# Performance work log

Hardware: AMD Instinct MI355X
Metric: run time of the kernel (lower is better)

## Reference

```python
import jax, jax.numpy as jnp
import numpy as np

EPS = 1e-5   # BatchNorm3d eps
SLOPE = 0.01 # LeakyReLU default negative_slope

def conv3(x, w, pad):
    return jax.lax.conv_general_dilated(
        x, w, (1, 1, 1), [(pad, pad)] * 3,
        dimension_numbers=('NCDHW', 'OIDHW', 'NCDHW'))

def bn(x):
    # BatchNorm3d in training mode with affine init (weight=1, bias=0):
    # normalize by per-channel batch statistics (biased variance).
    m = x.mean(axis=(0, 2, 3, 4), keepdims=True)
    v = x.var(axis=(0, 2, 3, 4), keepdims=True)
    return (x - m) / jnp.sqrt(v + EPS)

def lrelu(x):
    return jnp.where(x >= 0, x, SLOPE * x)

def block(x, w1, w2):
    # ConvBlock: conv3x3x3 -> BN -> LeakyReLU, twice
    x = lrelu(bn(conv3(x, w1, 1)))
    return lrelu(bn(conv3(x, w2, 1)))

def maxpool2(x):
    # MaxPool3dMPS(kernel=2, stride=2, pad=0) == standard 2x2x2 maxpool
    B, C, D, H, W = x.shape
    return x.reshape(B, C, D // 2, 2, H // 2, 2, W // 2, 2).max(axis=(3, 5, 7))

def upconv_fft(x, w):
    # ConvTranspose3dMPS: nearest-neighbor upsample by stride=2 via repeat,
    # then per-(out,in)-channel CIRCULAR convolution implemented with FFTs
    # (weight zero-padded to the upsampled spatial shape). Vectorized here
    # over all channel pairs with a frequency-domain einsum; rfft is used
    # since all signals are real (identical math, half the memory).
    s = 2
    B, C, D, H, W = x.shape
    up = jnp.broadcast_to(x[:, :, :, None, :, None, :, None],
                          (B, C, D, s, H, s, W, s)).reshape(B, C, D * s, H * s, W * s)
    sp = up.shape[2:]
    X = jnp.fft.rfftn(up, axes=(2, 3, 4))                 # [B, Cin, D', H', Wf]
    Wf = jnp.fft.rfftn(w, s=sp, axes=(2, 3, 4))           # [Cout, Cin, D', H', Wf]
    Y = jnp.einsum('bidhw,oidhw->bodhw', X, Wf)
    return jnp.fft.irfftn(Y, s=sp, axes=(2, 3, 4))

def unet_fwd(x, wf1, wf2, wd1a, wd1b, wd2a, wd2b, wd3a, wd3b,
             wt1, wu1a, wu1b, wt2, wu2a, wu2b, wt3, wu3a, wu3b,
             w_final, b_final):
    x1 = block(x, wf1, wf2)                       # [B,16,64,64,64]
    x2 = block(maxpool2(x1), wd1a, wd1b)          # [B,32,32,32,32]
    x3 = block(maxpool2(x2), wd2a, wd2b)          # [B,64,16,16,16]
    x4 = block(maxpool2(x3), wd3a, wd3b)          # [B,128,8,8,8]

    def up(a, skip, wt, wa, wb):
        u = lrelu(bn(upconv_fft(a, wt)))
        return block(jnp.concatenate([skip, u], axis=1), wa, wb)

    a = up(x4, x3, wt1, wu1a, wu1b)               # [B,64,16,16,16]
    a = up(a, x2, wt2, wu2a, wu2b)                # [B,32,32,32,32]
    a = up(a, x1, wt3, wu3a, wu3b)                # [B,16,64,64,64]
    return conv3(a, w_final, 0) + b_final.reshape(1, -1, 1, 1, 1)

def setup_inputs() -> dict:
    key = jax.random.key(0)
    ks = jax.random.split(key, 32)
    def W(k, shape):
        fan = int(np.prod(shape[1:]))
        return jax.random.normal(k, shape, jnp.float32) * np.float32((2.0 / fan) ** 0.5)
    inp = {}
    inp['x'] = jax.random.normal(ks[0], (1, 1, 64, 64, 64), jnp.float32)
    shapes = {
        'wf1': (16, 1, 3, 3, 3),  'wf2': (16, 16, 3, 3, 3),
        'wd1a': (32, 16, 3, 3, 3), 'wd1b': (32, 32, 3, 3, 3),
        'wd2a': (64, 32, 3, 3, 3), 'wd2b': (64, 64, 3, 3, 3),
        'wd3a': (128, 64, 3, 3, 3), 'wd3b': (128, 128, 3, 3, 3),
        'wt1': (64, 128, 2, 2, 2), 'wu1a': (64, 128, 3, 3, 3), 'wu1b': (64, 64, 3, 3, 3),
        'wt2': (32, 64, 2, 2, 2),  'wu2a': (32, 64, 3, 3, 3),  'wu2b': (32, 32, 3, 3, 3),
        'wt3': (16, 32, 2, 2, 2),  'wu3a': (16, 32, 3, 3, 3),  'wu3b': (16, 16, 3, 3, 3),
        'w_final': (1, 16, 1, 1, 1),
    }
    for i, (name, sh) in enumerate(shapes.items()):
        inp[name] = W(ks[i + 1], sh)
    inp['b_final'] = jnp.zeros((1,), jnp.float32)
    return inp

def reference(x, wf1, wf2, wd1a, wd1b, wd2a, wd2b, wd3a, wd3b,
              wt1, wu1a, wu1b, wt2, wu2a, wu2b, wt3, wu3a, wu3b,
              w_final, b_final):
    return unet_fwd(x, wf1, wf2, wd1a, wd1b, wd2a, wd2b, wd3a, wd3b,
                    wt1, wu1a, wu1b, wt2, wu2a, wu2b, wt3, wu3a, wu3b,
                    w_final, b_final)
```

## Files before the change

kernel.cpp:

```cpp
#include <hip/hip_runtime.h>

#define EPS   1e-5f
#define SLOPE 0.01f

template <int CIN>
__global__ __launch_bounds__(64) void conv3_big(const float* __restrict__ in,
                                                const float* __restrict__ wt,
                                                float* __restrict__ out,
                                                float* __restrict__ bstat) {
    const int V   = 64 * 64 * 64;
    const int NB  = gridDim.y;
    const int co0 = blockIdx.x * 8;
    __shared__ float tile[3][6][68];

    const int vb    = blockIdx.y * 256;
    const int d0    = vb >> 12;
    const int hbase = (vb >> 6) & 63;
    const int hh0   = threadIdx.x >> 4;
    const int w0    = (threadIdx.x & 15) * 4;
    const int v0    = vb + (hh0 * 64) + w0;
    const bool mL = (w0 != 0);
    const bool mR = (w0 + 4 != 64);

    int  goff[5];
    int  loff[5];
    bool gok[5];
    bool act[5];
#pragma unroll
    for (int t = 0; t < 5; ++t) {
        const int idx = threadIdx.x + t * 64;
        act[t] = (idx < 288);
        const int r  = idx >> 4;
        const int wq = (idx & 15) * 4;
        const int kd = r / 6;
        const int hh = r - kd * 6;
        const int zd = d0 + kd - 1;
        const int zh = hbase + hh - 1;
        gok[t]  = act[t] & ((unsigned)zd < 64u) & ((unsigned)zh < 64u);
        goff[t] = gok[t] ? ((zd << 6) + zh) * 64 + wq : 0;
        loff[t] = act[t] ? (kd * 6 + hh) * 68 + wq : 0;
    }

    float acc[32];
#pragma unroll
    for (int i = 0; i < 32; ++i) acc[i] = 0.f;

    float4 pre[5];
#pragma unroll
    for (int t = 0; t < 5; ++t) {
        float4 val = make_float4(0.f, 0.f, 0.f, 0.f);
        if (gok[t]) val = *(const float4*)(in + goff[t]);
        pre[t] = val;
    }

#pragma unroll 1
    for (int ci = 0; ci < CIN; ++ci) {
#pragma unroll
        for (int t = 0; t < 5; ++t)
            if (act[t]) *(float4*)&((float*)tile)[loff[t]] = pre[t];
        if (ci + 1 < CIN) {
            const float* pc = in + (size_t)(ci + 1) * V;
#pragma unroll
            for (int t = 0; t < 5; ++t) {
                float4 val = make_float4(0.f, 0.f, 0.f, 0.f);
                if (gok[t]) val = *(const float4*)(pc + goff[t]);
                pre[t] = val;
            }
        }
#pragma unroll 1
        for (int kd = 0; kd < 3; ++kd) {
#pragma unroll
            for (int kh = 0; kh < 3; ++kh) {
                const float* trow = &tile[kd][hh0 + kh][0];
                const float4 m = *(const float4*)(trow + w0);
                const float lv = mL ? trow[w0 - 1] : 0.f;
                const float rv = mR ? trow[w0 + 4] : 0.f;
                const float* wbase = wt + ((size_t)co0 * CIN + ci) * 27
                                        + (kd * 3 + kh) * 3;
#define FMA4C(A0, A1, A2, AP)                                                       \
                {                                                                   \
                    float* a = (AP);                                                \
                    a[0] = fmaf(lv,  (A0), fmaf(m.x, (A1), fmaf(m.y, (A2), a[0]))); \
                    a[1] = fmaf(m.x, (A0), fmaf(m.y, (A1), fmaf(m.z, (A2), a[1]))); \
                    a[2] = fmaf(m.y, (A0), fmaf(m.z, (A1), fmaf(m.w, (A2), a[2]))); \
                    a[3] = fmaf(m.z, (A0), fmaf(m.w, (A1), fmaf(rv,  (A2), a[3]))); \
                }
#pragma unroll
                for (int co = 0; co < 8; ++co) {
                    const float* wp = wbase + (size_t)co * (CIN * 27);
                    const float a0 = wp[0];
                    const float a1 = wp[1];
                    const float a2 = wp[2];
                    FMA4C(a0, a1, a2, acc + co * 4);
                }
#undef FMA4C
            }
        }
    }
#pragma unroll
    for (int co = 0; co < 8; ++co)
        *(float4*)&out[(size_t)(co0 + co) * V + v0] = *(const float4*)&acc[co * 4];

    float s1[8], s2[8];
#pragma unroll
    for (int co = 0; co < 8; ++co) {
        const float* a = &acc[co * 4];
        s1[co] = a[0] + a[1] + a[2] + a[3];
        s2[co] = fmaf(a[0], a[0], fmaf(a[1], a[1], fmaf(a[2], a[2], a[3] * a[3])));
    }
#pragma unroll
    for (int off = 32; off > 0; off >>= 1)
#pragma unroll
        for (int co = 0; co < 8; ++co) {
            s1[co] += __shfl_down(s1[co], off, 64);
            s2[co] += __shfl_down(s2[co], off, 64);
        }
    if (threadIdx.x == 0)
#pragma unroll
        for (int co = 0; co < 8; ++co) {
            bstat[((size_t)(co0 + co) * NB + blockIdx.y) * 2]     = s1[co];
            bstat[((size_t)(co0 + co) * NB + blockIdx.y) * 2 + 1] = s2[co];
        }
}

template <int CIN, int CC>
__global__ __launch_bounds__(128) void conv3_t32(const float* __restrict__ in,
                                                 const float* __restrict__ wt,
                                                 float* __restrict__ part) {
    const int V    = 32 * 32 * 32;
    const int Cout = gridDim.x * 8;
    const int z    = blockIdx.z;
    const int cib  = z * CC;
    __shared__ float wlds[27 * CC * 8];
    __shared__ float tile[3][18][36];
    const int co0 = blockIdx.x * 8;
    for (int i = threadIdx.x; i < 27 * CC * 8; i += 128) {
        const int co  = i & 7;
        const int r   = i >> 3;
        const int tap = r % 3;
        const int r2  = r / 3;
        const int pl  = r2 % 9;
        const int ci  = r2 / 9;
        wlds[i] = wt[((size_t)(co0 + co) * CIN + cib + ci) * 27 + pl * 3 + tap];
    }

    const int vb    = blockIdx.y * 512;
    const int d0    = vb >> 10;
    const int hbase = (vb >> 5) & 31;
    const int hh0   = threadIdx.x >> 3;
    const int w0    = (threadIdx.x & 7) * 4;
    const int v0    = vb + hh0 * 32 + w0;
    const bool mL = (w0 != 0);
    const bool mR = (w0 + 4 != 32);

    int  goff[4];
    int  loff[4];
    bool gok[4];
    bool act[4];
#pragma unroll
    for (int t = 0; t < 4; ++t) {
        const int idx = threadIdx.x + t * 128;
        act[t] = (idx < 432);
        const int r  = idx >> 3;
        const int wq = (idx & 7) * 4;
        const int kd = r / 18;
        const int hh = r - kd * 18;
        const int zd = d0 + kd - 1;
        const int zh = hbase + hh - 1;
        gok[t]  = act[t] & ((unsigned)zd < 32u) & ((unsigned)zh < 32u);
        goff[t] = gok[t] ? ((zd << 5) + zh) * 32 + wq : 0;
        loff[t] = act[t] ? (kd * 18 + hh) * 36 + wq : 0;
    }

    float acc[32];
#pragma unroll
    for (int i = 0; i < 32; ++i) acc[i] = 0.f;

    const float* inz = in + (size_t)cib * V;
    float4 pre[4];
#pragma unroll
    for (int t = 0; t < 4; ++t) {
        float4 val = make_float4(0.f, 0.f, 0.f, 0.f);
        if (gok[t]) val = *(const float4*)(inz + goff[t]);
        pre[t] = val;
    }

#pragma unroll 1
    for (int ci = 0; ci < CC; ++ci) {
        __syncthreads();
#pragma unroll
        for (int t = 0; t < 4; ++t)
            if (act[t]) *(float4*)&((float*)tile)[loff[t]] = pre[t];
        if (ci + 1 < CC) {
            const float* pc = inz + (size_t)(ci + 1) * V;
#pragma unroll
            for (int t = 0; t < 4; ++t) {
                float4 val = make_float4(0.f, 0.f, 0.f, 0.f);
                if (gok[t]) val = *(const float4*)(pc + goff[t]);
                pre[t] = val;
            }
        }
        __syncthreads();
#pragma unroll 1
        for (int kd = 0; kd < 3; ++kd) {
#pragma unroll
            for (int kh = 0; kh < 3; ++kh) {
                const float* trow = &tile[kd][hh0 + kh][0];
                const float4 m = *(const float4*)(trow + w0);
                const float lv = mL ? trow[w0 - 1] : 0.f;
                const float rv = mR ? trow[w0 + 4] : 0.f;
                const float* wb = &wlds[((ci * 9 + kd * 3 + kh) * 3) * 8];
                const float4 t0a = *(const float4*)(wb);
                const float4 t0b = *(const float4*)(wb + 4);
                const float4 t1a = *(const float4*)(wb + 8);
                const float4 t1b = *(const float4*)(wb + 12);
                const float4 t2a = *(const float4*)(wb + 16);
                const float4 t2b = *(const float4*)(wb + 20);
#define FMA4C(A0, A1, A2, AP)                                                       \
                {                                                                   \
                    float* a = (AP);                                                \
                    a[0] = fmaf(lv,  (A0), fmaf(m.x, (A1), fmaf(m.y, (A2), a[0]))); \
                    a[1] = fmaf(m.x, (A0), fmaf(m.y, (A1), fmaf(m.z, (A2), a[1]))); \
                    a[2] = fmaf(m.y, (A0), fmaf(m.z, (A1), fmaf(m.w, (A2), a[2]))); \
                    a[3] = fmaf(m.z, (A0), fmaf(m.w, (A1), fmaf(rv,  (A2), a[3]))); \
                }
                FMA4C(t0a.x, t1a.x, t2a.x, acc + 0);
                FMA4C(t0a.y, t1a.y, t2a.y, acc + 4);
                FMA4C(t0a.z, t1a.z, t2a.z, acc + 8);
                FMA4C(t0a.w, t1a.w, t2a.w, acc + 12);
                FMA4C(t0b.x, t1b.x, t2b.x, acc + 16);
                FMA4C(t0b.y, t1b.y, t2b.y, acc + 20);
                FMA4C(t0b.z, t1b.z, t2b.z, acc + 24);
                FMA4C(t0b.w, t1b.w, t2b.w, acc + 28);
#undef FMA4C
            }
        }
    }
#pragma unroll
    for (int co = 0; co < 8; ++co)
        *(float4*)&part[((size_t)z * Cout + co0 + co) * V + v0] = *(const float4*)&acc[co * 4];
}

template <int CIN>
__global__ __launch_bounds__(256) void upconv_big(const float* __restrict__ in,
                                                  const float* __restrict__ wt,
                                                  float* __restrict__ out,
                                                  float* __restrict__ bstat,
                                                  int Di, int Hi, int Wi) {
    const int Do = 2 * Di, Ho = 2 * Hi, Wo = 2 * Wi;
    const int Vo = Do * Ho * Wo;
    const int Vi = Di * Hi * Wi;
    const int NB = gridDim.y;
    const int co0 = blockIdx.x * 8;
    __shared__ float wlds[8 * CIN * 8];
    __shared__ float sred[4 * 16];
    for (int i = threadIdx.x; i < 8 * CIN * 8; i += 256) {
        const int co  = i & 7;
        const int t2  = i >> 3;
        const int ci  = t2 % CIN;
        const int tap = t2 / CIN;
        wlds[i] = wt[((size_t)(co0 + co) * CIN + ci) * 8 + tap];
    }
    __syncthreads();

    const int vbase = blockIdx.y * 1024 + threadIdx.x;
    int od[4], oh[4], ow[4];
#pragma unroll
    for (int j = 0; j < 4; ++j) {
        const int v = vbase + j * 256;
        ow[j] = v % Wo;
        oh[j] = (v / Wo) % Ho;
        od[j] = v / (Wo * Ho);
    }
    float acc[32];
#pragma unroll
    for (int i = 0; i < 32; ++i) acc[i] = 0.f;

#pragma unroll 1
    for (int kd = 0; kd < 2; ++kd)
#pragma unroll 1
    for (int kh = 0; kh < 2; ++kh)
#pragma unroll
    for (int kw = 0; kw < 2; ++kw) {
        const int tap = (kd * 2 + kh) * 2 + kw;
        int sp[4];
#pragma unroll
        for (int j = 0; j < 4; ++j) {
            const int id = ((od[j] - kd + Do) & (Do - 1)) >> 1;
            const int ih = ((oh[j] - kh + Ho) & (Ho - 1)) >> 1;
            const int iw = ((ow[j] - kw + Wo) & (Wo - 1)) >> 1;
            sp[j] = (id * Hi + ih) * Wi + iw;
        }
        const float* wrow = &wlds[tap * CIN * 8];
#pragma unroll 2
        for (int ci = 0; ci < CIN; ++ci) {
            float xv[4];
#pragma unroll
            for (int j = 0; j < 4; ++j)
                xv[j] = in[(size_t)ci * Vi + sp[j]];
            const float4 wa = *(const float4*)(wrow + ci * 8);
            const float4 wb = *(const float4*)(wrow + ci * 8 + 4);
#define UF(WC, CO)                                                              \
            {                                                                   \
                _Pragma("unroll")                                               \
                for (int j = 0; j < 4; ++j)                                     \
                    acc[(CO) * 4 + j] = fmaf(xv[j], (WC), acc[(CO) * 4 + j]);   \
            }
            UF(wa.x, 0) UF(wa.y, 1) UF(wa.z, 2) UF(wa.w, 3)
            UF(wb.x, 4) UF(wb.y, 5) UF(wb.z, 6) UF(wb.w, 7)
#undef UF
        }
    }
#pragma unroll
    for (int co = 0; co < 8; ++co)
#pragma unroll
        for (int j = 0; j < 4; ++j)
            out[(size_t)(co0 + co) * Vo + vbase + j * 256] = acc[co * 4 + j];

    float s1[8], s2[8];
#pragma unroll
    for (int co = 0; co < 8; ++co) {
        const float* a = &acc[co * 4];
        s1[co] = a[0] + a[1] + a[2] + a[3];
        s2[co] = fmaf(a[0], a[0], fmaf(a[1], a[1], fmaf(a[2], a[2], a[3] * a[3])));
    }
#pragma unroll
    for (int off = 32; off > 0; off >>= 1)
#pragma unroll
        for (int co = 0; co < 8; ++co) {
            s1[co] += __shfl_down(s1[co], off, 64);
            s2[co] += __shfl_down(s2[co], off, 64);
        }
    const int lane = threadIdx.x & 63;
    const int wv   = threadIdx.x >> 6;
    if (lane == 0)
#pragma unroll
        for (int co = 0; co < 8; ++co) {
            sred[(wv * 8 + co) * 2]     = s1[co];
            sred[(wv * 8 + co) * 2 + 1] = s2[co];
        }
    __syncthreads();
    if ((int)threadIdx.x < 8) {
        float S1 = 0.f, S2 = 0.f;
#pragma unroll
        for (int w = 0; w < 4; ++w) {
            S1 += sred[(w * 8 + threadIdx.x) * 2];
            S2 += sred[(w * 8 + threadIdx.x) * 2 + 1];
        }
        bstat[((size_t)(co0 + threadIdx.x) * NB + blockIdx.y) * 2]     = S1;
        bstat[((size_t)(co0 + threadIdx.x) * NB + blockIdx.y) * 2 + 1] = S2;
    }
}

__global__ __launch_bounds__(256) void bn_apply_f(const float* __restrict__ prt,
                                                  float* __restrict__ dst,
                                                  const float* __restrict__ bstat,
                                                  int NB, int V4, float invV) {
    const int c = blockIdx.x;
    float s1 = 0.f, s2 = 0.f;
    for (int i = threadIdx.x; i < NB; i += 256) {
        s1 += bstat[((size_t)c * NB + i) * 2];
        s2 += bstat[((size_t)c * NB + i) * 2 + 1];
    }
#pragma unroll
    for (int off = 32; off > 0; off >>= 1) {
        s1 += __shfl_down(s1, off, 64);
        s2 += __shfl_down(s2, off, 64);
    }
    __shared__ float sh[8];
    __shared__ float mv[2];
    const int lane = threadIdx.x & 63;
    const int wv   = threadIdx.x >> 6;
    if (lane == 0) { sh[wv] = s1; sh[4 + wv] = s2; }
    __syncthreads();
    if (threadIdx.x == 0) {
        const float S1 = sh[0] + sh[1] + sh[2] + sh[3];
        const float S2 = sh[4] + sh[5] + sh[6] + sh[7];
        const float mean = S1 * invV;
        const float var  = S2 * invV - mean * mean;
        mv[0] = mean;
        mv[1] = rsqrtf(var + EPS);
    }
    __syncthreads();
    const float mean = mv[0];
    const float rstd = mv[1];
    const int pos = blockIdx.y * 256 + threadIdx.x;
    float4 t = ((const float4*)prt)[(size_t)c * V4 + pos];
    float u;
    u = (t.x - mean) * rstd; t.x = u >= 0.f ? u : SLOPE * u;
    u = (t.y - mean) * rstd; t.y = u >= 0.f ? u : SLOPE * u;
    u = (t.z - mean) * rstd; t.z = u >= 0.f ? u : SLOPE * u;
    u = (t.w - mean) * rstd; t.w = u >= 0.f ? u : SLOPE * u;
    ((float4*)dst)[(size_t)c * V4 + pos] = t;
}

template <int CIN, int CC, int BT>
__global__ __launch_bounds__(BT) void conv3_qA(const float* __restrict__ in,
                                               const float* __restrict__ wt,
                                               float* __restrict__ part,
                                               int D, int H, int W) {
    const int V    = D * H * W;
    const int Cout = gridDim.x * 8;
    const int z    = blockIdx.z;
    const int cib  = z * CC;
    __shared__ float wlds[27 * CC * 8];
    const int co0 = blockIdx.x * 8;
    for (int i = threadIdx.x; i < 27 * CC * 8; i += BT) {
        const int co  = i & 7;
        const int t2  = i >> 3;
        const int tap = t2 % 3;
        const int t3  = t2 / 3;
        const int ci  = t3 % CC;
        const int pl  = t3 / CC;
        wlds[i] = wt[((size_t)(co0 + co) * CIN + cib + ci) * 27 + pl * 3 + tap];
    }
    __syncthreads();

    const float* inz = in + (size_t)cib * V;
    const int v0 = (blockIdx.y * BT + threadIdx.x) * 4;
    const int w0 = v0 % W;
    const int h0 = (v0 / W) % H;
    const int d0 = v0 / (W * H);

    const bool mL = (w0 != 0);
    const bool mR = (w0 + 4 != W);
    const int  wl = w0 - (mL ? 1 : 0);
    const int  wr = w0 + (mR ? 4 : 3);

    float acc[32];
#pragma unroll
    for (int i = 0; i < 32; ++i) acc[i] = 0.f;

#pragma unroll 1
    for (int kd = 0; kd < 3; ++kd) {
#pragma unroll 1
        for (int kh = 0; kh < 3; ++kh) {
            const int zd = d0 + kd - 1, zh = h0 + kh - 1;
            const bool okp = ((unsigned)zd < (unsigned)D) & ((unsigned)zh < (unsigned)H);
            const int row = okp ? (zd * H + zh) * W : 0;
            const float* wpl = &wlds[(kd * 3 + kh) * CC * 24];
#pragma unroll 2
            for (int ci = 0; ci < CC; ++ci) {
                const float* p = inz + (size_t)ci * V + row;
                float4 m = *(const float4*)(p + w0);
                float lv = p[wl];
                float rv = p[wr];
                if (!okp) { m.x = 0.f; m.y = 0.f; m.z = 0.f; m.w = 0.f; }
                if (!(okp && mL)) lv = 0.f;
                if (!(okp && mR)) rv = 0.f;
                const float* wb = wpl + ci * 24;
                const float4 t0a = *(const float4*)(wb);
                const float4 t0b = *(const float4*)(wb + 4);
                const float4 t1a = *(const float4*)(wb + 8);
                const float4 t1b = *(const float4*)(wb + 12);
                const float4 t2a = *(const float4*)(wb + 16);
                const float4 t2b = *(const float4*)(wb + 20);
#define FMA4C(A0, A1, A2, AP)                                                       \
                {                                                                   \
                    float* a = (AP);                                                \
                    a[0] = fmaf(lv,  (A0), fmaf(m.x, (A1), fmaf(m.y, (A2), a[0]))); \
                    a[1] = fmaf(m.x, (A0), fmaf(m.y, (A1), fmaf(m.z, (A2), a[1]))); \
                    a[2] = fmaf(m.y, (A0), fmaf(m.z, (A1), fmaf(m.w, (A2), a[2]))); \
                    a[3] = fmaf(m.z, (A0), fmaf(m.w, (A1), fmaf(rv,  (A2), a[3]))); \
                }
                FMA4C(t0a.x, t1a.x, t2a.x, acc + 0);
                FMA4C(t0a.y, t1a.y, t2a.y, acc + 4);
                FMA4C(t0a.z, t1a.z, t2a.z, acc + 8);
                FMA4C(t0a.w, t1a.w, t2a.w, acc + 12);
                FMA4C(t0b.x, t1b.x, t2b.x, acc + 16);
                FMA4C(t0b.y, t1b.y, t2b.y, acc + 20);
                FMA4C(t0b.z, t1b.z, t2b.z, acc + 24);
                FMA4C(t0b.w, t1b.w, t2b.w, acc + 28);
#undef FMA4C
            }
        }
    }
#pragma unroll
    for (int co = 0; co < 8; ++co)
        *(float4*)&part[((size_t)z * Cout + co0 + co) * V + v0] = *(const float4*)&acc[co * 4];
}

template <int CIN, int CC, int VOXB>
__global__ __launch_bounds__(256) void upconv_v8(const float* __restrict__ in,
                                                 const float* __restrict__ wt,
                                                 float* __restrict__ part,
                                                 int Di, int Hi, int Wi) {
    const int Do = 2 * Di, Ho = 2 * Hi, Wo = 2 * Wi;
    const int Vo = Do * Ho * Wo;
    const int Vi = Di * Hi * Wi;
    const int Cout = gridDim.x * 8;
    const int z    = blockIdx.z;
    const int cib  = z * CC;
    __shared__ float wlds[8 * CC * 8];
    const int co0 = blockIdx.x * 8;
    for (int i = threadIdx.x; i < 8 * CC * 8; i += 256) {
        const int co  = i & 7;
        const int t2  = i >> 3;
        const int ci  = t2 % CC;
        const int tap = t2 / CC;
        wlds[i] = wt[((size_t)(co0 + co) * CIN + cib + ci) * 8 + tap];
    }
    __syncthreads();

    const float* inz = in + (size_t)cib * Vi;
    const int vbase = blockIdx.y * (256 * VOXB) + threadIdx.x;
    int od[VOXB], oh[VOXB], ow[VOXB];
#pragma unroll
    for (int j = 0; j < VOXB; ++j) {
        const int v = vbase + j * 256;
        ow[j] = v % Wo;
        oh[j] = (v / Wo) % Ho;
        od[j] = v / (Wo * Ho);
    }
    float acc[8 * VOXB];
#pragma unroll
    for (int i = 0; i < 8 * VOXB; ++i) acc[i] = 0.f;

#pragma unroll 1
    for (int kd = 0; kd < 2; ++kd)
#pragma unroll 1
    for (int kh = 0; kh < 2; ++kh)
#pragma unroll
    for (int kw = 0; kw < 2; ++kw) {
        const int tap = (kd * 2 + kh) * 2 + kw;
        int sp[VOXB];
#pragma unroll
        for (int j = 0; j < VOXB; ++j) {
            const int id = ((od[j] - kd + Do) & (Do - 1)) >> 1;
            const int ih = ((oh[j] - kh + Ho) & (Ho - 1)) >> 1;
            const int iw = ((ow[j] - kw + Wo) & (Wo - 1)) >> 1;
            sp[j] = (id * Hi + ih) * Wi + iw;
        }
        const float* wrow = &wlds[tap * CC * 8];
#pragma unroll 2
        for (int ci = 0; ci < CC; ++ci) {
            float xv[VOXB];
#pragma unroll
            for (int j = 0; j < VOXB; ++j)
                xv[j] = inz[(size_t)ci * Vi + sp[j]];
            const float4 wa = *(const float4*)(wrow + ci * 8);
            const float4 wb = *(const float4*)(wrow + ci * 8 + 4);
#define UF(WC, CO)                                                              \
            {                                                                   \
                _Pragma("unroll")                                               \
                for (int j = 0; j < VOXB; ++j)                                  \
                    acc[(CO) * VOXB + j] = fmaf(xv[j], (WC), acc[(CO) * VOXB + j]); \
            }
            UF(wa.x, 0) UF(wa.y, 1) UF(wa.z, 2) UF(wa.w, 3)
            UF(wb.x, 4) UF(wb.y, 5) UF(wb.z, 6) UF(wb.w, 7)
#undef UF
        }
    }
#pragma unroll
    for (int co = 0; co < 8; ++co)
#pragma unroll
        for (int j = 0; j < VOXB; ++j)
            part[((size_t)z * Cout + co0 + co) * Vo + vbase + j * 256] = acc[co * VOXB + j];
}

__global__ __launch_bounds__(256) void bn_stats_part_v2(const float* __restrict__ part,
                                                        float* __restrict__ pstat,
                                                        int C, int V, int S, int chunk) {
    const int c = blockIdx.x, seg = blockIdx.y;
    const size_t base = (size_t)c * V + (size_t)seg * chunk;
    float s1 = 0.f, s2 = 0.f;
    for (int i = threadIdx.x * 4; i < chunk; i += 1024) {
        float4 t = make_float4(0.f, 0.f, 0.f, 0.f);
        for (int s = 0; s < S; ++s) {
            const float4 v = *(const float4*)(part + (size_t)s * C * V + base + i);
            t.x += v.x; t.y += v.y; t.z += v.z; t.w += v.w;
        }
        s1 += t.x + t.y + t.z + t.w;
        s2 = fmaf(t.x, t.x, fmaf(t.y, t.y, fmaf(t.z, t.z, fmaf(t.w, t.w, s2))));
    }
#pragma unroll
    for (int off = 32; off > 0; off >>= 1) {
        s1 += __shfl_down(s1, off, 64);
        s2 += __shfl_down(s2, off, 64);
    }
    __shared__ float sh[8];
    const int wid  = threadIdx.x >> 6;
    const int lane = threadIdx.x & 63;
    if (lane == 0) { sh[wid] = s1; sh[4 + wid] = s2; }
    __syncthreads();
    if (threadIdx.x == 0) {
        pstat[(c * gridDim.y + seg) * 2]     = sh[0] + sh[1] + sh[2] + sh[3];
        pstat[(c * gridDim.y + seg) * 2 + 1] = sh[4] + sh[5] + sh[6] + sh[7];
    }
}

__global__ __launch_bounds__(256) void bn_apply_v4(const float* __restrict__ part,
                                                   float* __restrict__ dst,
                                                   const float* __restrict__ pstat,
                                                   int C, int V4, int S, int NSEG,
                                                   float invV, int total4) {
    const int idx = blockIdx.x * blockDim.x + threadIdx.x;
    if (idx >= total4) return;
    const int c = idx / V4;
    const int v = idx - c * V4;
    float s1 = 0.f, s2 = 0.f;
    for (int g = 0; g < NSEG; ++g) {
        s1 += pstat[(c * NSEG + g) * 2];
        s2 += pstat[(c * NSEG + g) * 2 + 1];
    }
    const float mean = s1 * invV;
    const float var  = s2 * invV - mean * mean;
    const float rstd = rsqrtf(var + EPS);
    const float4* p4 = (const float4*)part;
    float4 t = make_float4(0.f, 0.f, 0.f, 0.f);
    for (int s = 0; s < S; ++s) {
        const float4 x = p4[(size_t)(s * C + c) * V4 + v];
        t.x += x.x; t.y += x.y; t.z += x.z; t.w += x.w;
    }
    float u;
    u = (t.x - mean) * rstd; t.x = u >= 0.f ? u : SLOPE * u;
    u = (t.y - mean) * rstd; t.y = u >= 0.f ? u : SLOPE * u;
    u = (t.z - mean) * rstd; t.z = u >= 0.f ? u : SLOPE * u;
    u = (t.w - mean) * rstd; t.w = u >= 0.f ? u : SLOPE * u;
    ((float4*)dst)[idx] = t;
}

__global__ __launch_bounds__(256) void maxpool_kernel(const float* __restrict__ in,
                                                      float* __restrict__ out,
                                                      int D, int H, int W, int total) {
    const int Do = D >> 1, Ho = H >> 1, Wo = W >> 1;
    const int Vo = Do * Ho * Wo;
    const int idx = blockIdx.x * blockDim.x + threadIdx.x;
    if (idx >= total) return;
    const int c  = idx / Vo;
    const int v  = idx - c * Vo;
    const int ow = v % Wo;
    const int oh = (v / Wo) % Ho;
    const int od = v / (Wo * Ho);
    const size_t HW = (size_t)H * W;
    const float* p = in + (size_t)c * D * HW + (size_t)(2 * od) * HW + (size_t)(2 * oh) * W + 2 * ow;
    float m = p[0];
    m = fmaxf(m, p[1]);
    m = fmaxf(m, p[W]);
    m = fmaxf(m, p[W + 1]);
    m = fmaxf(m, p[HW]);
    m = fmaxf(m, p[HW + 1]);
    m = fmaxf(m, p[HW + W]);
    m = fmaxf(m, p[HW + W + 1]);
    out[idx] = m;
}

__global__ __launch_bounds__(256) void final_v2(const float* __restrict__ in,
                                                const float* __restrict__ w,
                                                const float* __restrict__ b,
                                                float* __restrict__ out, int C, int V4) {
    const int idx = blockIdx.x * blockDim.x + threadIdx.x;
    if (idx >= V4) return;
    const float bb = b[0];
    float4 acc = make_float4(bb, bb, bb, bb);
    for (int c = 0; c < C; ++c) {
        const float4 v = ((const float4*)in)[(size_t)c * V4 + idx];
        const float wc = w[c];
        acc.x = fmaf(v.x, wc, acc.x);
        acc.y = fmaf(v.y, wc, acc.y);
        acc.z = fmaf(v.z, wc, acc.z);
        acc.w = fmaf(v.w, wc, acc.w);
    }
    ((float4*)out)[idx] = acc;
}


extern "C" void kernel_launch(void* const* d_in, const int* in_sizes, int n_in,
                              void* d_out, int out_size, void* d_ws, size_t ws_size,
                              hipStream_t stream) {
    const float* x      = (const float*)d_in[0];
    const float* wf1    = (const float*)d_in[1];
    const float* wf2    = (const float*)d_in[2];
    const float* wd1a   = (const float*)d_in[3];
    const float* wd1b   = (const float*)d_in[4];
    const float* wd2a   = (const float*)d_in[5];
    const float* wd2b   = (const float*)d_in[6];
    const float* wd3a   = (const float*)d_in[7];
    const float* wd3b   = (const float*)d_in[8];
    const float* wt1    = (const float*)d_in[9];
    const float* wu1a   = (const float*)d_in[10];
    const float* wu1b   = (const float*)d_in[11];
    const float* wt2    = (const float*)d_in[12];
    const float* wu2a   = (const float*)d_in[13];
    const float* wu2b   = (const float*)d_in[14];
    const float* wt3    = (const float*)d_in[15];
    const float* wu3a   = (const float*)d_in[16];
    const float* wu3b   = (const float*)d_in[17];
    const float* w_fin  = (const float*)d_in[18];
    const float* b_fin  = (const float*)d_in[19];
    float* out = (float*)d_out;

    const int V0 = 64 * 64 * 64;
    const int V1 = 32 * 32 * 32;
    const int V2 = 16 * 16 * 16;
    const int V3 = 8 * 8 * 8;

    float* ws    = (float*)d_ws;
    float* cat3  = ws;
    float* cat2  = cat3 + (size_t)32 * V0;
    float* cat1  = cat2 + (size_t)64 * V1;
    float* x4    = cat1 + (size_t)128 * V2;
    float* tA    = x4   + (size_t)128 * V3;
    float* tB    = tA   + (size_t)16 * V0;
    float* part  = tB   + (size_t)16 * V0;
    float* pstat = part + (size_t)16 * V0;
    float* bstat = pstat + 4096;

    auto blocks = [](int n) { return (n + 255) / 256; };

    auto bn_lrelu = [&](const float* p, float* dstp, int C, int V, int S) {
        const int NSEG = (V >= V0) ? 16 : (V == V1) ? 8 : (V == V2) ? 2 : 1;
        hipLaunchKernelGGL(bn_stats_part_v2, dim3(C, NSEG), dim3(256), 0, stream,
                           p, pstat, C, V, S, V / NSEG);
        const int total4 = C * V / 4;
        hipLaunchKernelGGL(bn_apply_v4, dim3(blocks(total4)), dim3(256), 0, stream,
                           p, dstp, pstat, C, V / 4, S, NSEG, 1.f / V, total4);
    };
    auto maxpool = [&](const float* in, float* o, int C, int D, int H, int W) {
        const int total = C * (D / 2) * (H / 2) * (W / 2);
        hipLaunchKernelGGL(maxpool_kernel, dim3(blocks(total)), dim3(256), 0, stream,
                           in, o, D, H, W, total);
    };

#define CONVBIG(CIN, in_, wt_, prt_, dst_, Cout)                                            \
    {                                                                                       \
        const int NBv = V0 / 256;                                                           \
        dim3 g((Cout) / 8, NBv);                                                            \
        hipLaunchKernelGGL((conv3_big<CIN>), g, dim3(64), 0, stream,                        \
                           in_, wt_, prt_, bstat);                                          \
        hipLaunchKernelGGL(bn_apply_f, dim3(Cout, V0 / 4 / 256), dim3(256), 0, stream,      \
                           prt_, dst_, bstat, NBv, V0 / 4, 1.f / V0);                       \
    }
#define CONVT32(CIN, CC, in_, wt_, prt_, dst_, Cout)                                        \
    {                                                                                       \
        const int S = (CIN) / (CC);                                                         \
        dim3 g((Cout) / 8, V1 / 512, S);                                                    \
        hipLaunchKernelGGL((conv3_t32<CIN, CC>), g, dim3(128), 0, stream,                   \
                           in_, wt_, prt_);                                                 \
        bn_lrelu(prt_, dst_, Cout, V1, S);                                                  \
    }
#define CONVQ(CIN, CC, BT, in_, wt_, prt_, dst_, Cout, D_, H_, W_)                          \
    {                                                                                       \
        const int V_ = (D_) * (H_) * (W_);                                                  \
        const int S  = (CIN) / (CC);                                                        \
        dim3 g((Cout) / 8, V_ / (4 * (BT)), S);                                             \
        hipLaunchKernelGGL((conv3_qA<CIN, CC, BT>), g, dim3(BT), 0, stream,                 \
                           in_, wt_, prt_, D_, H_, W_);                                     \
        bn_lrelu(prt_, dst_, Cout, V_, S);                                                  \
    }
#define UPCONV(CIN, CC, VOXB, in_, wt_, prt_, dst_, Cout, Di_, Hi_, Wi_)                    \
    {                                                                                       \
        const int Vo_ = 8 * (Di_) * (Hi_) * (Wi_);                                          \
        const int S  = (CIN) / (CC);                                                        \
        dim3 g((Cout) / 8, Vo_ / (256 * (VOXB)), S);                                        \
        hipLaunchKernelGGL((upconv_v8<CIN, CC, VOXB>), g, dim3(256), 0, stream,             \
                           in_, wt_, prt_, Di_, Hi_, Wi_);                                  \
        bn_lrelu(prt_, dst_, Cout, Vo_, S);                                                 \
    }

    CONVBIG(1,  x,  wf1, tA, tA,   16);
    CONVBIG(16, tA, wf2, tB, cat3, 16);
    maxpool(cat3, tA, 16, 64, 64, 64);
    CONVT32(16,  8, tA,  wd1a, part, tB,   32);
    CONVT32(32,  8, tB,  wd1b, part, cat2, 32);
    maxpool(cat2, tA, 32, 32, 32, 32);
    CONVQ(32,  8,  64,  tA,  wd2a, part, tB,          64, 16, 16, 16);
    CONVQ(64,  8,  64,  tB,  wd2b, part, cat1,        64, 16, 16, 16);
    maxpool(cat1, tA, 64, 16, 16, 16);
    CONVQ(64,  4,  64,  tA,  wd3a, part, tB,         128, 8, 8, 8);
    CONVQ(128, 8,  64,  tB,  wd3b, part, x4,         128, 8, 8, 8);

    UPCONV(128, 16, 1, x4, wt1, part, cat1 + (size_t)64 * V2, 64, 8, 8, 8);
    CONVQ(128, 8,  64, cat1, wu1a, part, tA,          64, 16, 16, 16);
    CONVQ(64,  8,  64, tA,   wu1b, part, tB,          64, 16, 16, 16);

    UPCONV(64, 16, 1, tB, wt2, part, cat2 + (size_t)32 * V1, 32, 16, 16, 16);
    CONVT32(64, 16, cat2, wu2a, part, tA, 32);
    CONVT32(32, 8,  tA,   wu2b, part, tB, 32);

    {
        float* up3dst = cat3 + (size_t)16 * V0;
        const int NBv = V0 / 1024;
        dim3 g(2, NBv);
        hipLaunchKernelGGL((upconv_big<32>), g, dim3(256), 0, stream,
                           tB, wt3, up3dst, bstat, 32, 32, 32);
        hipLaunchKernelGGL(bn_apply_f, dim3(16, V0 / 4 / 256), dim3(256), 0, stream,
                           up3dst, up3dst, bstat, NBv, V0 / 4, 1.f / V0);
    }
    CONVBIG(32, cat3, wu3a, tB,   tA, 16);
    CONVBIG(16, tA,   wu3b, cat3, tB, 16);

    hipLaunchKernelGGL(final_v2, dim3(blocks(V0 / 4)), dim3(256), 0, stream,
                       tB, w_fin, b_fin, out, 16, V0 / 4);

#undef CONVBIG
#undef CONVT32
#undef CONVQ
#undef UPCONV
}
```

Baseline: 950.4 us.

## Split input channels across two wavefronts in full-resolution conv with LDS reduction

The 64x64x64 conv kernel now takes a wavefront count template parameter. With two waves, each wave handles half of the input channels in its own LDS tile, and partial accumulators are summed through shared memory before the store and the BN statistics reduction. This shortens the serial per-block channel loop and adds more waves per block to hide latency. The cost is extra LDS (tile copies plus a 32x64 reduction buffer), a block barrier, and half the threads idling during the epilogue.

```diff
diff --git a/kernel.cpp b/kernel.cpp
--- a/kernel.cpp
+++ b/kernel.cpp
@@ -3,21 +3,27 @@
 #define EPS   1e-5f
 #define SLOPE 0.01f
 
-template <int CIN>
-__global__ __launch_bounds__(64) void conv3_big(const float* __restrict__ in,
-                                                const float* __restrict__ wt,
-                                                float* __restrict__ out,
-                                                float* __restrict__ bstat) {
+template <int CIN, int NW>
+__global__ __launch_bounds__(64 * NW) void conv3_big(const float* __restrict__ in,
+                                                     const float* __restrict__ wt,
+                                                     float* __restrict__ out,
+                                                     float* __restrict__ bstat) {
     const int V   = 64 * 64 * 64;
     const int NB  = gridDim.y;
     const int co0 = blockIdx.x * 8;
-    __shared__ float tile[3][6][68];
+    constexpr int CPW = CIN / NW;
+    __shared__ float tile[NW][3][6][68];
+    __shared__ float red[(NW > 1) ? 32 * 64 : 1];
+
+    const int wv   = threadIdx.x >> 6;
+    const int lane = threadIdx.x & 63;
+    const int cbeg = wv * CPW;
 
     const int vb    = blockIdx.y * 256;
     const int d0    = vb >> 12;
     const int hbase = (vb >> 6) & 63;
-    const int hh0   = threadIdx.x >> 4;
-    const int w0    = (threadIdx.x & 15) * 4;
+    const int hh0   = lane >> 4;
+    const int w0    = (lane & 15) * 4;
     const int v0    = vb + (hh0 * 64) + w0;
     const bool mL = (w0 != 0);
     const bool mR = (w0 + 4 != 64);
@@ -28,7 +34,7 @@
     bool act[5];
 #pragma unroll
     for (int t = 0; t < 5; ++t) {
-        const int idx = threadIdx.x + t * 64;
+        const int idx = lane + t * 64;
         act[t] = (idx < 288);
         const int r  = idx >> 4;
         const int wq = (idx & 15) * 4;
@@ -40,26 +46,31 @@
         goff[t] = gok[t] ? ((zd << 6) + zh) * 64 + wq : 0;
         loff[t] = act[t] ? (kd * 6 + hh) * 68 + wq : 0;
     }
+    float* mytile = &tile[wv][0][0][0];
 
     float acc[32];
 #pragma unroll
     for (int i = 0; i < 32; ++i) acc[i] = 0.f;
 
     float4 pre[5];
-#pragma unroll
-    for (int t = 0; t < 5; ++t) {
-        float4 val = make_float4(0.f, 0.f, 0.f, 0.f);
-        if (gok[t]) val = *(const float4*)(in + goff[t]);
-        pre[t] = val;
-    }
-
-#pragma unroll 1
-    for (int ci = 0; ci < CIN; ++ci) {
+    {
+        const float* pc = in + (size_t)cbeg * V;
+#pragma unroll
+        for (int t = 0; t < 5; ++t) {
+            float4 val = make_float4(0.f, 0.f, 0.f, 0.f);
+            if (gok[t]) val = *(const float4*)(pc + goff[t]);
+            pre[t] = val;
+        }
+    }
+
+#pragma unroll 1
+    for (int ci = 0; ci < CPW; ++ci) {
+        const int c = cbeg + ci;
 #pragma unroll
         for (int t = 0; t < 5; ++t)
-            if (act[t]) *(float4*)&((float*)tile)[loff[t]] = pre[t];
-        if (ci + 1 < CIN) {
-            const float* pc = in + (size_t)(ci + 1) * V;
+            if (act[t]) *(float4*)&mytile[loff[t]] = pre[t];
+        if (ci + 1 < CPW) {
+            const float* pc = in + (size_t)(c + 1) * V;
 #pragma unroll
             for (int t = 0; t < 5; ++t) {
                 float4 val = make_float4(0.f, 0.f, 0.f, 0.f);
@@ -71,11 +82,11 @@
         for (int kd = 0; kd < 3; ++kd) {
 #pragma unroll
             for (int kh = 0; kh < 3; ++kh) {
-                const float* trow = &tile[kd][hh0 + kh][0];
+                const float* trow = &mytile[(kd * 6 + hh0 + kh) * 68];
                 const float4 m = *(const float4*)(trow + w0);
                 const float lv = mL ? trow[w0 - 1] : 0.f;
                 const float rv = mR ? trow[w0 + 4] : 0.f;
-                const float* wbase = wt + ((size_t)co0 * CIN + ci) * 27
+                const float* wbase = wt + ((size_t)co0 * CIN + c) * 27
                                         + (kd * 3 + kh) * 3;
 #define FMA4C(A0, A1, A2, AP)                                                       \
                 {                                                                   \
@@ -97,30 +108,46 @@
             }
         }
     }
-#pragma unroll
-    for (int co = 0; co < 8; ++co)
-        *(float4*)&out[(size_t)(co0 + co) * V + v0] = *(const float4*)&acc[co * 4];
-
-    float s1[8], s2[8];
-#pragma unroll
-    for (int co = 0; co < 8; ++co) {
-        const float* a = &acc[co * 4];
-        s1[co] = a[0] + a[1] + a[2] + a[3];
-        s2[co] = fmaf(a[0], a[0], fmaf(a[1], a[1], fmaf(a[2], a[2], a[3] * a[3])));
-    }
-#pragma unroll
-    for (int off = 32; off > 0; off >>= 1)
+
+    if (NW > 1) {
+        if (wv == 1) {
+#pragma unroll
+            for (int i = 0; i < 32; ++i)
+                red[i * 64 + lane] = acc[i];
+        }
+        __syncthreads();
+        if (wv == 0) {
+#pragma unroll
+            for (int i = 0; i < 32; ++i)
+                acc[i] += red[i * 64 + lane];
+        }
+    }
+    if (wv == 0) {
+#pragma unroll
+        for (int co = 0; co < 8; ++co)
+            *(float4*)&out[(size_t)(co0 + co) * V + v0] = *(const float4*)&acc[co * 4];
+
+        float s1[8], s2[8];
 #pragma unroll
         for (int co = 0; co < 8; ++co) {
-            s1[co] += __shfl_down(s1[co], off, 64);
-            s2[co] += __shfl_down(s2[co], off, 64);
-        }
-    if (threadIdx.x == 0)
-#pragma unroll
-        for (int co = 0; co < 8; ++co) {
-            bstat[((size_t)(co0 + co) * NB + blockIdx.y) * 2]     = s1[co];
-            bstat[((size_t)(co0 + co) * NB + blockIdx.y) * 2 + 1] = s2[co];
-        }
+            const float* a = &acc[co * 4];
+            s1[co] = a[0] + a[1] + a[2] + a[3];
+            s2[co] = fmaf(a[0], a[0], fmaf(a[1], a[1], fmaf(a[2], a[2], a[3] * a[3])));
+        }
+#pragma unroll
+        for (int off = 32; off > 0; off >>= 1)
+#pragma unroll
+            for (int co = 0; co < 8; ++co) {
+                s1[co] += __shfl_down(s1[co], off, 64);
+                s2[co] += __shfl_down(s2[co], off, 64);
+            }
+        if (lane == 0)
+#pragma unroll
+            for (int co = 0; co < 8; ++co) {
+                bstat[((size_t)(co0 + co) * NB + blockIdx.y) * 2]     = s1[co];
+                bstat[((size_t)(co0 + co) * NB + blockIdx.y) * 2 + 1] = s2[co];
+            }
+    }
 }
 
 template <int CIN, int CC>
@@ -722,11 +749,11 @@
                            in, o, D, H, W, total);
     };
 
-#define CONVBIG(CIN, in_, wt_, prt_, dst_, Cout)                                            \
+#define CONVBIG(CIN, NW, in_, wt_, prt_, dst_, Cout)                                        \
     {                                                                                       \
         const int NBv = V0 / 256;                                                           \
         dim3 g((Cout) / 8, NBv);                                                            \
-        hipLaunchKernelGGL((conv3_big<CIN>), g, dim3(64), 0, stream,                        \
+        hipLaunchKernelGGL((conv3_big<CIN, NW>), g, dim3(64 * (NW)), 0, stream,             \
                            in_, wt_, prt_, bstat);                                          \
         hipLaunchKernelGGL(bn_apply_f, dim3(Cout, V0 / 4 / 256), dim3(256), 0, stream,      \
                            prt_, dst_, bstat, NBv, V0 / 4, 1.f / V0);                       \
@@ -758,8 +785,8 @@
         bn_lrelu(prt_, dst_, Cout, Vo_, S);                                                 \
     }
 
-    CONVBIG(1,  x,  wf1, tA, tA,   16);
-    CONVBIG(16, tA, wf2, tB, cat3, 16);
+    CONVBIG(1,  1, x,  wf1, tA, tA,   16);
+    CONVBIG(16, 2, tA, wf2, tB, cat3, 16);
     maxpool(cat3, tA, 16, 64, 64, 64);
     CONVT32(16,  8, tA,  wd1a, part, tB,   32);
     CONVT32(32,  8, tB,  wd1b, part, cat2, 32);
@@ -787,8 +814,8 @@
         hipLaunchKernelGGL(bn_apply_f, dim3(16, V0 / 4 / 256), dim3(256), 0, stream,
                            up3dst, up3dst, bstat, NBv, V0 / 4, 1.f / V0);
     }
-    CONVBIG(32, cat3, wu3a, tB,   tA, 16);
-    CONVBIG(16, tA,   wu3b, cat3, tB, 16);
+    CONVBIG(32, 2, cat3, wu3a, tB, tA, 16);
+    CONVBIG(16, 2, tA,   wu3b, cat3, tB, 16);
 
     hipLaunchKernelGGL(final_v2, dim3(blocks(V0 / 4)), dim3(256), 0, stream,
                        tB, w_fin, b_fin, out, 16, V0 / 4);
```

Measured after the change: 1.047 ms. 1.1x slower.
